# Kernel optimization log

Hardware: AMD Instinct MI355X
Metric: run time of the kernel (lower is better)

The kernel has to match this reference:

```python
import jax, jax.numpy as jnp
import numpy as np

B, DIN, HID, COMP = 16384, 1024, 512, 64

def setup_inputs() -> dict:
    key = jax.random.key(0)
    ks = jax.random.split(key, 16)
    s = lambda fan_in: 1.0 / np.sqrt(fan_in)
    return {
        "x1": jax.random.normal(ks[0], (B, DIN), jnp.float32),
        "x2": jax.random.normal(ks[1], (B, DIN), jnp.float32),
        "Wb1": jax.random.normal(ks[2], (DIN, HID), jnp.float32) * s(DIN),
        "bb1": jnp.zeros((HID,), jnp.float32),
        "Wb2": jax.random.normal(ks[3], (DIN, HID), jnp.float32) * s(DIN),
        "bb2": jnp.zeros((HID,), jnp.float32),
        "Wc1": jax.random.normal(ks[4], (HID, COMP), jnp.float32) * s(HID),
        "bc1": jnp.zeros((COMP,), jnp.float32),
        "Wc2": jax.random.normal(ks[5], (HID, COMP), jnp.float32) * s(HID),
        "bc2": jnp.zeros((COMP,), jnp.float32),
        "Wf1": jax.random.normal(ks[6], (COMP * COMP, 64), jnp.float32) * s(COMP * COMP),
        "bf1": jnp.zeros((64,), jnp.float32),
        "Wf2": jax.random.normal(ks[7], (64, 2), jnp.float32) * s(64),
        "bf2": jnp.zeros((2,), jnp.float32),
    }

def reference(x1, x2, Wb1, bb1, Wb2, bb2, Wc1, bc1, Wc2, bc2, Wf1, bf1, Wf2, bf2):
    # branch + compress: [B, DIN] -> [B, HID] -> [B, COMP]
    f1 = (jax.nn.relu(x1 @ Wb1 + bb1)) @ Wc1 + bc1  # [B, 64]
    f2 = (jax.nn.relu(x2 @ Wb2 + bb2)) @ Wc2 + bc2  # [B, 64]
    # kronecker_product(f1, f2): per-sample (f2 col) * (f1 row) -> [64,64], row-major flatten
    # element at flat index p*64 + q is f2[p] * f1[q]
    kron = jnp.einsum('bp,bq->bpq', f2, f1).reshape(f1.shape[0], -1)  # [B, 4096]
    h = kron @ Wf1 + bf1   # [B, 64]
    out = h @ Wf2 + bf2    # [B, 2]
    return out
```

## Files before the change

kernel.cpp:

```cpp
#include <hip/hip_runtime.h>

#define B_SZ 16384
#define DIN  1024
#define HID  512
#define COMP 64

typedef __bf16 bf16_t;
typedef __bf16 bf16x4 __attribute__((ext_vector_type(4)));
typedef __bf16 bf16x8 __attribute__((ext_vector_type(8)));
typedef float  f32x4  __attribute__((ext_vector_type(4)));

#define MFMA16 __builtin_amdgcn_mfma_f32_16x16x32_bf16

__device__ __forceinline__ void gl2lds16(const void* g, void* l) {
    __builtin_amdgcn_global_load_lds(
        (const __attribute__((address_space(1))) void*)g,
        (__attribute__((address_space(3))) void*)l, 16, 0, 0);
}

__device__ __forceinline__ bf16x8 cvt8(float4 a, float4 b) {
    bf16x8 o;
    o[0] = (bf16_t)a.x; o[1] = (bf16_t)a.y;
    o[2] = (bf16_t)a.z; o[3] = (bf16_t)a.w;
    o[4] = (bf16_t)b.x; o[5] = (bf16_t)b.y;
    o[6] = (bf16_t)b.z; o[7] = (bf16_t)b.w;
    return o;
}

__global__ __launch_bounds__(256) void k_prep(
    const float* __restrict__ Wb1, const float* __restrict__ Wb2,
    bf16_t* __restrict__ wbt1, bf16_t* __restrict__ wbt2,
    const float* __restrict__ Wc1, const float* __restrict__ Wc2,
    bf16_t* __restrict__ wct1, bf16_t* __restrict__ wct2,
    const float* __restrict__ Wf1, const float* __restrict__ bf1v,
    const float* __restrict__ Wf2, const float* __restrict__ bf2v,
    const float* __restrict__ bc1, const float* __restrict__ bc2,
    float* __restrict__ f1, float* __restrict__ f2,
    float* __restrict__ G, float* __restrict__ c)
{
    const int bid = blockIdx.x, tid = threadIdx.x;

    __shared__ float tile[32][33];
    const int tx = tid & 31, ty = tid >> 5;

    if (bid < 1024) {
        const int z = bid >> 9, t = bid & 511;
        const float* in  = z ? Wb2  : Wb1;
        bf16_t*      out = z ? wbt2 : wbt1;
        const int n0 = (t & 15) * 32, k0 = (t >> 4) * 32;
        #pragma unroll
        for (int i = 0; i < 4; i++)
            tile[ty + i * 8][tx] = in[(size_t)(k0 + ty + i * 8) * HID + n0 + tx];
        __syncthreads();
        #pragma unroll
        for (int i = 0; i < 4; i++)
            out[(size_t)(n0 + ty + i * 8) * DIN + k0 + tx] = (bf16_t)tile[tx][ty + i * 8];
    } else if (bid < 1088) {
        const int l = bid - 1024;
        const int z = l >> 5, t = l & 31;
        const float* in  = z ? Wc2  : Wc1;
        bf16_t*      out = z ? wct2 : wct1;
        const int n0 = (t & 1) * 32, k0 = (t >> 1) * 32;
        #pragma unroll
        for (int i = 0; i < 4; i++)
            tile[ty + i * 8][tx] = in[(size_t)(k0 + ty + i * 8) * COMP + n0 + tx];
        __syncthreads();
        #pragma unroll
        for (int i = 0; i < 4; i++)
            out[(size_t)(n0 + ty + i * 8) * HID + k0 + tx] = (bf16_t)tile[tx][ty + i * 8];
    } else if (bid < 1104) {
        const int i = (bid - 1088) * 256 + tid;
        float a0 = 0.f, a1 = 0.f;
        #pragma unroll 8
        for (int o = 0; o < 64; o++) {
            float w = Wf1[(size_t)i * 64 + o];
            a0 = fmaf(w, Wf2[o * 2 + 0], a0);
            a1 = fmaf(w, Wf2[o * 2 + 1], a1);
        }
        G[i]        = a0;
        G[4096 + i] = a1;
        if (i < 2) {
            float s = bf2v[i];
            for (int o = 0; o < 64; o++) s = fmaf(bf1v[o], Wf2[o * 2 + i], s);
            c[i] = s;
        }
    } else {
        const int l = bid - 1104;
        const int z = l >> 10;
        const float* bc = z ? bc2 : bc1;
        float*       f  = z ? f2  : f1;
        const int i = (l & 1023) * 256 + tid;
        const int c4 = (i & 15) * 4;
        float4 v = make_float4(bc[c4], bc[c4 + 1], bc[c4 + 2], bc[c4 + 3]);
        reinterpret_cast<float4*>(f)[i] = v;
    }
}

__global__ __launch_bounds__(256, 2) void k_gemm1f(
    const float* __restrict__ X1, const float* __restrict__ X2,
    const bf16_t* __restrict__ WT1, const bf16_t* __restrict__ WT2,
    const float* __restrict__ bias1, const float* __restrict__ bias2,
    const bf16_t* __restrict__ WC1, const bf16_t* __restrict__ WC2,
    float* __restrict__ F1, float* __restrict__ F2)
{
    const int bid = blockIdx.x;
    const int nid = (bid & 7) * 128 + (bid >> 3);
    const int z   = nid >> 9;
    const int r9  = nid & 511;
    const int mb  = r9 >> 2;
    const int nb  = r9 & 3;

    const float*  X    = z ? X2    : X1;
    const bf16_t* WT   = z ? WT2   : WT1;
    const float*  bias = z ? bias2 : bias1;
    const bf16_t* WC   = z ? WC2   : WC1;
    float*        F    = z ? F2    : F1;

    const int m0 = mb * 128;
    const int n0 = nb * 128;

    __shared__ __align__(128) char smem[65536];

    const int tid  = threadIdx.x;
    const int lane = tid & 63;
    const int wave = tid >> 6;
    const int wm   = wave >> 1;
    const int wn   = wave & 1;
    const int l15  = lane & 15;
    const int g4   = lane >> 4;

    const int srow = tid >> 3;
    const int sc   = (tid & 7) ^ (srow & 7);
    const float*  gX = X  + (size_t)(m0 + srow) * DIN + sc * 8;
    const bf16_t* gB = WT + (size_t)(n0 + srow) * DIN + sc * 8;
    const int ldst = tid * 16;

    const int l7   = l15 & 7;
    const int lch0 = (g4 ^ l7) * 16;
    const int lch1 = ((4 + g4) ^ l7) * 16;
    const int abase = (wm * 64 + l15) * 128;
    const int bbase = (wn * 64 + l15) * 128;

    f32x4  acc[4][4] = {};
    float4 r[8];

    #pragma unroll
    for (int i = 0; i < 4; i++) {
        r[2*i]   = *(const float4*)(gX + (size_t)i * 32 * DIN);
        r[2*i+1] = *(const float4*)(gX + (size_t)i * 32 * DIN + 4);
    }
    #pragma unroll
    for (int i = 0; i < 4; i++)
        gl2lds16(gB + (size_t)i * 32 * DIN, smem + 32768 + i * 4096 + ldst);
    #pragma unroll
    for (int i = 0; i < 4; i++)
        *(bf16x8*)(smem + i * 4096 + ldst) = cvt8(r[2*i], r[2*i+1]);
    #pragma unroll
    for (int i = 0; i < 4; i++) {
        r[2*i]   = *(const float4*)(gX + (size_t)i * 32 * DIN + 64);
        r[2*i+1] = *(const float4*)(gX + (size_t)i * 32 * DIN + 64 + 4);
    }
    __builtin_amdgcn_sched_barrier(0);
    asm volatile("s_waitcnt vmcnt(8) lgkmcnt(0)" ::: "memory");
    __builtin_amdgcn_s_barrier();
    __builtin_amdgcn_sched_barrier(0);

    #pragma unroll 1
    for (int kt = 0; kt < 16; ++kt) {
        const int d = kt & 1;
        const char* Ac = smem + d * 16384;
        const char* Bc = smem + 32768 + d * 16384;
        char* An = (char*)smem + (d ^ 1) * 16384;
        char* Bn = (char*)smem + 32768 + (d ^ 1) * 16384;
        const int kc1 = (kt < 15 ? kt + 1 : 15) * 64;
        const int kc2 = (kt < 14 ? kt + 2 : 15) * 64;

        #pragma unroll
        for (int i = 0; i < 4; i++)
            gl2lds16(gB + (size_t)i * 32 * DIN + kc1, Bn + i * 4096 + ldst);
        __builtin_amdgcn_sched_barrier(0);

        bf16x8 a[4][2], b[4][2];
        #pragma unroll
        for (int mi = 0; mi < 4; mi++) {
            a[mi][0] = *(const bf16x8*)(Ac + abase + mi * 2048 + lch0);
            a[mi][1] = *(const bf16x8*)(Ac + abase + mi * 2048 + lch1);
        }
        #pragma unroll
        for (int ni = 0; ni < 4; ni++) {
            b[ni][0] = *(const bf16x8*)(Bc + bbase + ni * 2048 + lch0);
            b[ni][1] = *(const bf16x8*)(Bc + bbase + ni * 2048 + lch1);
        }
        __builtin_amdgcn_s_setprio(1);
        #pragma unroll
        for (int mi = 0; mi < 4; mi++)
            #pragma unroll
            for (int ni = 0; ni < 4; ni++) {
                acc[mi][ni] = MFMA16(a[mi][0], b[ni][0], acc[mi][ni], 0, 0, 0);
                acc[mi][ni] = MFMA16(a[mi][1], b[ni][1], acc[mi][ni], 0, 0, 0);
            }
        __builtin_amdgcn_s_setprio(0);
        __builtin_amdgcn_sched_barrier(0);

        #pragma unroll
        for (int i = 0; i < 4; i++)
            *(bf16x8*)(An + i * 4096 + ldst) = cvt8(r[2*i], r[2*i+1]);
        __builtin_amdgcn_sched_barrier(0);
        #pragma unroll
        for (int i = 0; i < 4; i++) {
            r[2*i]   = *(const float4*)(gX + (size_t)i * 32 * DIN + kc2);
            r[2*i+1] = *(const float4*)(gX + (size_t)i * 32 * DIN + kc2 + 4);
        }
        __builtin_amdgcn_sched_barrier(0);

        asm volatile("s_waitcnt vmcnt(8) lgkmcnt(0)" ::: "memory");
        __builtin_amdgcn_s_barrier();
        __builtin_amdgcn_sched_barrier(0);
    }

    asm volatile("s_waitcnt vmcnt(0) lgkmcnt(0)" ::: "memory");
    __builtin_amdgcn_s_barrier();

    bf16_t* Hs = (bf16_t*)smem;
    float bv[4];
    #pragma unroll
    for (int ni = 0; ni < 4; ni++)
        bv[ni] = bias[n0 + wn * 64 + ni * 16 + l15];
    #pragma unroll
    for (int mi = 0; mi < 4; mi++) {
        const int lr = wm * 64 + mi * 16 + g4 * 4;
        #pragma unroll
        for (int ni = 0; ni < 4; ni++) {
            const int colL = wn * 64 + ni * 16 + l15;
            #pragma unroll
            for (int rr = 0; rr < 4; rr++) {
                float v = fmaxf(acc[mi][ni][rr] + bv[ni], 0.0f);
                Hs[(lr + rr) * 136 + colL] = (bf16_t)v;
            }
        }
    }
    __syncthreads();

    f32x4 acc2[2][4] = {};
    #pragma unroll
    for (int kk = 0; kk < 128; kk += 32) {
        bf16x8 af2[2];
        #pragma unroll
        for (int m2 = 0; m2 < 2; m2++)
            af2[m2] = *(const bf16x8*)(Hs + (wave * 32 + m2 * 16 + l15) * 136 + kk + g4 * 8);
        #pragma unroll
        for (int ni = 0; ni < 4; ni++) {
            bf16x8 bw = *(const bf16x8*)(&WC[(size_t)(ni * 16 + l15) * HID + n0 + kk + g4 * 8]);
            #pragma unroll
            for (int m2 = 0; m2 < 2; m2++)
                acc2[m2][ni] = MFMA16(af2[m2], bw, acc2[m2][ni], 0, 0, 0);
        }
    }
    #pragma unroll
    for (int m2 = 0; m2 < 2; m2++) {
        const int rbase = m0 + wave * 32 + m2 * 16 + g4 * 4;
        #pragma unroll
        for (int ni = 0; ni < 4; ni++) {
            const int col = ni * 16 + l15;
            #pragma unroll
            for (int rr = 0; rr < 4; rr++)
                unsafeAtomicAdd(&F[(size_t)(rbase + rr) * COMP + col], acc2[m2][ni][rr]);
        }
    }
}

__global__ __launch_bounds__(256) void k_bilinear(
    const float* __restrict__ f1, const float* __restrict__ f2,
    const float* __restrict__ G, const float* __restrict__ c,
    float* __restrict__ out)
{
    __shared__ float Gs[2][4096];
    __shared__ float f1t[64][66];
    __shared__ float f2t[64][66];
    __shared__ float part[4][64];

    const int tid = threadIdx.x;
    const int s0  = blockIdx.x * 64;

    for (int i = tid; i < 2048; i += 256)
        reinterpret_cast<float4*>(&Gs[0][0])[i] =
            reinterpret_cast<const float4*>(G)[i];

    #pragma unroll
    for (int rr = 0; rr < 4; rr++) {
        const int row = (tid >> 4) + rr * 16;
        const int c4  = (tid & 15) * 4;
        float4 v1 = *reinterpret_cast<const float4*>(&f1[(size_t)(s0 + row) * 64 + c4]);
        float4 v2 = *reinterpret_cast<const float4*>(&f2[(size_t)(s0 + row) * 64 + c4]);
        f1t[c4 + 0][row] = v1.x; f1t[c4 + 1][row] = v1.y;
        f1t[c4 + 2][row] = v1.z; f1t[c4 + 3][row] = v1.w;
        f2t[c4 + 0][row] = v2.x; f2t[c4 + 1][row] = v2.y;
        f2t[c4 + 2][row] = v2.z; f2t[c4 + 3][row] = v2.w;
    }
    __syncthreads();

    const int lane = tid & 63;
    const int wv   = tid >> 6;
    const int j    = wv & 1;
    const int qh   = (wv >> 1) * 32;

    float tq[32];
    #pragma unroll
    for (int q = 0; q < 32; q++) tq[q] = 0.f;

    #pragma unroll 4
    for (int p = 0; p < 64; p++) {
        const float f2p = f2t[p][lane];
        const float* Gp = &Gs[j][p * 64 + qh];
        #pragma unroll
        for (int q4 = 0; q4 < 8; q4++) {
            float4 g = *reinterpret_cast<const float4*>(Gp + q4 * 4);
            tq[q4 * 4 + 0] = fmaf(f2p, g.x, tq[q4 * 4 + 0]);
            tq[q4 * 4 + 1] = fmaf(f2p, g.y, tq[q4 * 4 + 1]);
            tq[q4 * 4 + 2] = fmaf(f2p, g.z, tq[q4 * 4 + 2]);
            tq[q4 * 4 + 3] = fmaf(f2p, g.w, tq[q4 * 4 + 3]);
        }
    }

    float o = 0.f;
    #pragma unroll
    for (int q = 0; q < 32; q++)
        o = fmaf(f1t[qh + q][lane], tq[q], o);

    part[wv][lane] = o;
    __syncthreads();

    if (wv < 2) {
        float r = part[wv][lane] + part[wv + 2][lane] + c[wv];
        out[(size_t)(s0 + lane) * 2 + wv] = r;
    }
}

extern "C" void kernel_launch(void* const* d_in, const int* in_sizes, int n_in,
                              void* d_out, int out_size, void* d_ws, size_t ws_size,
                              hipStream_t stream)
{
    const float* x1  = (const float*)d_in[0];
    const float* x2  = (const float*)d_in[1];
    const float* Wb1 = (const float*)d_in[2];
    const float* bb1 = (const float*)d_in[3];
    const float* Wb2 = (const float*)d_in[4];
    const float* bb2 = (const float*)d_in[5];
    const float* Wc1 = (const float*)d_in[6];
    const float* bc1 = (const float*)d_in[7];
    const float* Wc2 = (const float*)d_in[8];
    const float* bc2 = (const float*)d_in[9];
    const float* Wf1 = (const float*)d_in[10];
    const float* bf1v = (const float*)d_in[11];
    const float* Wf2 = (const float*)d_in[12];
    const float* bf2v = (const float*)d_in[13];
    float* out = (float*)d_out;

    char* ws = (char*)d_ws;
    bf16_t* wbt1 = (bf16_t*)ws; ws += (size_t)HID * DIN * 2;
    bf16_t* wbt2 = (bf16_t*)ws; ws += (size_t)HID * DIN * 2;
    bf16_t* wct1 = (bf16_t*)ws; ws += (size_t)COMP * HID * 2;
    bf16_t* wct2 = (bf16_t*)ws; ws += (size_t)COMP * HID * 2;
    float*  f1   = (float*)ws;  ws += (size_t)B_SZ * COMP * 4;
    float*  f2   = (float*)ws;  ws += (size_t)B_SZ * COMP * 4;
    float*  G    = (float*)ws;  ws += (size_t)2 * 4096 * 4;
    float*  c    = (float*)ws;  ws += 256;

    k_prep<<<3152, 256, 0, stream>>>(Wb1, Wb2, wbt1, wbt2,
                                     Wc1, Wc2, wct1, wct2,
                                     Wf1, bf1v, Wf2, bf2v,
                                     bc1, bc2, f1, f2, G, c);
    k_gemm1f<<<1024, 256, 0, stream>>>(x1, x2, wbt1, wbt2, bb1, bb2,
                                       wct1, wct2, f1, f2);
    k_bilinear<<<256, 256, 0, stream>>>(f1, f2, G, c, out);
}
```

Before: 238.8 us.

## Single-buffer LDS in first GEMM to fit four blocks per CU

The double-buffered A/B LDS staging in the fused first-GEMM kernel becomes a single buffer. Each k-step now converts and stores the prefetched X tile, issues the weight load, prefetches the next X slice, then synchronises before the MFMA work. The ReLU-hidden staging stride is cut from 136 to 132 so LDS fits in 33 KB. Launch bounds move from 2 to 4 blocks per CU, aiming to raise occupancy and hide latency across blocks rather than within one. In exchange the load/compute overlap inside a block is lost and there is an extra barrier per iteration. The tighter register budget with 64 accumulators could cause spills, and the 132 stride breaks 16-byte alignment of the bf16x8 LDS reads.

```diff
diff --git a/kernel.cpp b/kernel.cpp
--- a/kernel.cpp
+++ b/kernel.cpp
@@ -96,7 +96,7 @@
     }
 }
 
-__global__ __launch_bounds__(256, 2) void k_gemm1f(
+__global__ __launch_bounds__(256, 4) void k_gemm1f(
     const float* __restrict__ X1, const float* __restrict__ X2,
     const bf16_t* __restrict__ WT1, const bf16_t* __restrict__ WT2,
     const float* __restrict__ bias1, const float* __restrict__ bias2,
@@ -109,7 +109,6 @@
     const int r9  = nid & 511;
     const int mb  = r9 >> 2;
     const int nb  = r9 & 3;
-
     const float*  X    = z ? X2    : X1;
     const bf16_t* WT   = z ? WT2   : WT1;
     const float*  bias = z ? bias2 : bias1;
@@ -119,7 +118,7 @@
     const int m0 = mb * 128;
     const int n0 = nb * 128;
 
-    __shared__ __align__(128) char smem[65536];
+    __shared__ __align__(128) char smem[33792];
 
     const int tid  = threadIdx.x;
     const int lane = tid & 63;
@@ -149,47 +148,41 @@
         r[2*i]   = *(const float4*)(gX + (size_t)i * 32 * DIN);
         r[2*i+1] = *(const float4*)(gX + (size_t)i * 32 * DIN + 4);
     }
-    #pragma unroll
-    for (int i = 0; i < 4; i++)
-        gl2lds16(gB + (size_t)i * 32 * DIN, smem + 32768 + i * 4096 + ldst);
-    #pragma unroll
-    for (int i = 0; i < 4; i++)
-        *(bf16x8*)(smem + i * 4096 + ldst) = cvt8(r[2*i], r[2*i+1]);
-    #pragma unroll
-    for (int i = 0; i < 4; i++) {
-        r[2*i]   = *(const float4*)(gX + (size_t)i * 32 * DIN + 64);
-        r[2*i+1] = *(const float4*)(gX + (size_t)i * 32 * DIN + 64 + 4);
-    }
-    __builtin_amdgcn_sched_barrier(0);
-    asm volatile("s_waitcnt vmcnt(8) lgkmcnt(0)" ::: "memory");
-    __builtin_amdgcn_s_barrier();
     __builtin_amdgcn_sched_barrier(0);
 
     #pragma unroll 1
     for (int kt = 0; kt < 16; ++kt) {
-        const int d = kt & 1;
-        const char* Ac = smem + d * 16384;
-        const char* Bc = smem + 32768 + d * 16384;
-        char* An = (char*)smem + (d ^ 1) * 16384;
-        char* Bn = (char*)smem + 32768 + (d ^ 1) * 16384;
+        const int kc  = kt * 64;
         const int kc1 = (kt < 15 ? kt + 1 : 15) * 64;
-        const int kc2 = (kt < 14 ? kt + 2 : 15) * 64;
-
-        #pragma unroll
-        for (int i = 0; i < 4; i++)
-            gl2lds16(gB + (size_t)i * 32 * DIN + kc1, Bn + i * 4096 + ldst);
+
+        #pragma unroll
+        for (int i = 0; i < 4; i++)
+            *(bf16x8*)(smem + i * 4096 + ldst) = cvt8(r[2*i], r[2*i+1]);
+        __builtin_amdgcn_sched_barrier(0);
+        #pragma unroll
+        for (int i = 0; i < 4; i++)
+            gl2lds16(gB + (size_t)i * 32 * DIN + kc, smem + 16384 + i * 4096 + ldst);
+        __builtin_amdgcn_sched_barrier(0);
+        #pragma unroll
+        for (int i = 0; i < 4; i++) {
+            r[2*i]   = *(const float4*)(gX + (size_t)i * 32 * DIN + kc1);
+            r[2*i+1] = *(const float4*)(gX + (size_t)i * 32 * DIN + kc1 + 4);
+        }
+        __builtin_amdgcn_sched_barrier(0);
+        asm volatile("s_waitcnt vmcnt(8) lgkmcnt(0)" ::: "memory");
+        __builtin_amdgcn_s_barrier();
         __builtin_amdgcn_sched_barrier(0);
 
         bf16x8 a[4][2], b[4][2];
         #pragma unroll
         for (int mi = 0; mi < 4; mi++) {
-            a[mi][0] = *(const bf16x8*)(Ac + abase + mi * 2048 + lch0);
-            a[mi][1] = *(const bf16x8*)(Ac + abase + mi * 2048 + lch1);
+            a[mi][0] = *(const bf16x8*)(smem + abase + mi * 2048 + lch0);
+            a[mi][1] = *(const bf16x8*)(smem + abase + mi * 2048 + lch1);
         }
         #pragma unroll
         for (int ni = 0; ni < 4; ni++) {
-            b[ni][0] = *(const bf16x8*)(Bc + bbase + ni * 2048 + lch0);
-            b[ni][1] = *(const bf16x8*)(Bc + bbase + ni * 2048 + lch1);
+            b[ni][0] = *(const bf16x8*)(smem + 16384 + bbase + ni * 2048 + lch0);
+            b[ni][1] = *(const bf16x8*)(smem + 16384 + bbase + ni * 2048 + lch1);
         }
         __builtin_amdgcn_s_setprio(1);
         #pragma unroll
@@ -201,19 +194,6 @@
             }
         __builtin_amdgcn_s_setprio(0);
         __builtin_amdgcn_sched_barrier(0);
-
-        #pragma unroll
-        for (int i = 0; i < 4; i++)
-            *(bf16x8*)(An + i * 4096 + ldst) = cvt8(r[2*i], r[2*i+1]);
-        __builtin_amdgcn_sched_barrier(0);
-        #pragma unroll
-        for (int i = 0; i < 4; i++) {
-            r[2*i]   = *(const float4*)(gX + (size_t)i * 32 * DIN + kc2);
-            r[2*i+1] = *(const float4*)(gX + (size_t)i * 32 * DIN + kc2 + 4);
-        }
-        __builtin_amdgcn_sched_barrier(0);
-
-        asm volatile("s_waitcnt vmcnt(8) lgkmcnt(0)" ::: "memory");
         __builtin_amdgcn_s_barrier();
         __builtin_amdgcn_sched_barrier(0);
     }
@@ -235,7 +215,7 @@
             #pragma unroll
             for (int rr = 0; rr < 4; rr++) {
                 float v = fmaxf(acc[mi][ni][rr] + bv[ni], 0.0f);
-                Hs[(lr + rr) * 136 + colL] = (bf16_t)v;
+                Hs[(lr + rr) * 132 + colL] = (bf16_t)v;
             }
         }
     }
@@ -247,7 +227,7 @@
         bf16x8 af2[2];
         #pragma unroll
         for (int m2 = 0; m2 < 2; m2++)
-            af2[m2] = *(const bf16x8*)(Hs + (wave * 32 + m2 * 16 + l15) * 136 + kk + g4 * 8);
+            af2[m2] = *(const bf16x8*)(Hs + (wave * 32 + m2 * 16 + l15) * 132 + kk + g4 * 8);
         #pragma unroll
         for (int ni = 0; ni < 4; ni++) {
             bf16x8 bw = *(const bf16x8*)(&WC[(size_t)(ni * 16 + l15) * HID + n0 + kk + g4 * 8]);
```

New measurement: 505.6 us. 112% more time.
